# Performance work log

Measured on AMD Instinct MI355X. Metric: run time of the kernel, lower is better.

The kernel has to match this reference:

```python
import jax, jax.numpy as jnp
import numpy as np

DIM = 256
N_NODES = 2000
BATCH = 64


def _build_tree(n, seed=0):
    # Contiguous-children encoding: struct[i] = (ch_start, ch_end) or (-1,-1) for leaves.
    # Children indices are always > parent index (BFS frontier allocation).
    rng = np.random.default_rng(seed)
    struct = np.full((n, 2), -1, dtype=np.int32)
    ptr = 1
    i = 0
    while ptr < n:
        k = int(rng.integers(0, 5))
        if i + 1 >= ptr:  # keep the frontier non-empty
            k = max(k, 1)
        k = min(k, n - ptr)
        if k > 0:
            struct[i] = (ptr, ptr + k)
            ptr += k
        i += 1
    return struct


def _level_schedule(struct):
    # depth 0 = leaves; parent depth = 1 + max(child depths). Children idx > parent idx.
    n = struct.shape[0]
    depth = np.zeros(n, dtype=np.int64)
    for i in range(n - 1, -1, -1):
        s, e = struct[i]
        if s != -1:
            depth[i] = 1 + depth[s:e].max()
    return [np.nonzero(depth == d)[0] for d in range(int(depth.max()) + 1)]


def setup_inputs() -> dict:
    key = jax.random.key(0)
    ks = jax.random.split(key, 3)
    struct = _build_tree(N_NODES)
    structure = jnp.asarray(np.broadcast_to(struct, (BATCH, N_NODES, 2)).copy())
    features = jax.random.normal(ks[0], (BATCH, N_NODES, DIM), dtype=jnp.float32)
    s_in = (2.0 / (DIM + DIM)) ** 0.5        # glorot-ish scale
    s_inner = (2.0 / (3 * DIM + DIM)) ** 0.5
    W_in = jax.random.normal(ks[1], (DIM, DIM), dtype=jnp.float32) * s_in
    b_in = jnp.zeros((DIM,), jnp.float32)
    W_inner = jax.random.normal(ks[2], (3 * DIM, DIM), dtype=jnp.float32) * s_inner
    b_inner = jnp.zeros((DIM,), jnp.float32)
    return {"structure": structure, "features": features, "W_in": W_in,
            "b_in": b_in, "W_inner": W_inner, "b_inner": b_inner}


def reference(structure, features, W_in, b_in, W_inner, b_inner):
    # Tree structure (int) is a compile-time constant: derive a level schedule host-side,
    # then run one batched segment-reduction + Dense per tree level (deepest first).
    struct = np.asarray(structure[0])  # shared across batch
    levels = _level_schedule(struct)
    B, N, dim = features.shape
    state = jnp.zeros((B, N, dim), features.dtype)

    # Leaves: sigmoid Dense on own features (all features are finite/valid here).
    leaves = levels[0]
    state = state.at[:, leaves].set(jax.nn.sigmoid(features[:, leaves] @ W_in + b_in))

    for nodes in levels[1:]:
        starts, ends = struct[nodes, 0], struct[nodes, 1]
        counts = ends - starts
        child_ids = np.concatenate([np.arange(s, e) for s, e in zip(starts, ends)])
        seg = np.repeat(np.arange(len(nodes)), counts)
        L = len(nodes)
        cs = state[:, child_ids].transpose(1, 0, 2)          # [C, B, dim]
        ssum = jax.ops.segment_sum(cs, seg, num_segments=L)  # [L, B, dim]
        smin = jax.ops.segment_min(cs, seg, num_segments=L)
        feat = features[:, nodes].transpose(1, 0, 2)         # node's own feature joins pooling
        cnt = jnp.asarray(counts + 1, features.dtype)[:, None, None]
        c_mean = (ssum + feat) / cnt
        c_min = jnp.minimum(smin, feat)
        # NOTE: the source computes c_max with reduce_mean (bug) -> kept for fidelity.
        h = jnp.concatenate([c_mean, c_mean, c_min], axis=-1)  # [L, B, 3*dim]
        new = jax.nn.sigmoid(h @ W_inner + b_inner)
        state = state.at[:, nodes].set(new.transpose(1, 0, 2))

    return state[:, 0]  # just_root_output=True -> [B, dim]
```

## Files before the change

### kernel.cpp

```cpp
#include <hip/hip_runtime.h>

#define NNODES 2000
#define BATCH  64
#define DIM    256
#define BLOCK  256
#define MAXGRID 512
#define MAXLVL 128
#define TBLD   264

typedef __attribute__((ext_vector_type(8))) short  v8s;
typedef __attribute__((ext_vector_type(8))) __bf16 v8bf;
typedef __attribute__((ext_vector_type(4))) float  v4f;
typedef __attribute__((ext_vector_type(4))) int    v4i;

__device__ __forceinline__ short f2bf(float f) {
  unsigned u = __builtin_bit_cast(unsigned, f);
  u += 0x7FFFu + ((u >> 16) & 1u);
  return (short)(u >> 16);
}
__device__ __forceinline__ float bf2f(short s) {
  unsigned u = ((unsigned)(unsigned short)s) << 16;
  return __builtin_bit_cast(float, u);
}
__device__ __forceinline__ v4f mfma16(v8s a, v8s b, v4f c) {
  return __builtin_amdgcn_mfma_f32_16x16x32_bf16(
      __builtin_bit_cast(v8bf, a), __builtin_bit_cast(v8bf, b), c, 0, 0, 0);
}
__device__ __forceinline__ float sigmoidf(float x) {
  return __builtin_amdgcn_rcpf(1.0f + __builtin_amdgcn_exp2f(-1.4426950408889634f * x));
}

__global__ void prep1_kernel(const float* __restrict__ W_in, const float* __restrict__ W_inner,
                             short* __restrict__ Wt_in, short* __restrict__ Wt_inner,
                             int* __restrict__ bar) {
  int idx = blockIdx.x * blockDim.x + threadIdx.x;
  int stride = gridDim.x * blockDim.x;
  for (int i = idx; i < 256 * 256; i += stride) {
    int j = i >> 8, k = i & 255;
    Wt_in[j * 256 + k] = f2bf(W_in[k * 256 + j]);
  }
  for (int i = idx; i < 256 * 512; i += stride) {
    int j = i >> 9, k = i & 511;
    float v = W_inner[(k + 256) * 256 + j];
    if (k < 256) v += W_inner[k * 256 + j];
    Wt_inner[j * 512 + k] = f2bf(v);
  }
  if (idx == 0)
    __hip_atomic_store(bar, 0, __ATOMIC_RELAXED, __HIP_MEMORY_SCOPE_AGENT);
}

__global__ void prep2_kernel(const int* __restrict__ structure,
                             int* __restrict__ order, int* __restrict__ lstart,
                             int* __restrict__ meta) {
  __shared__ int   structS[NNODES * 2];
  __shared__ short h[NNODES];
  __shared__ int   counts[MAXLVL];
  __shared__ int   lsS[MAXLVL + 1];
  __shared__ int   chg, Hlev;
  const int tid = threadIdx.x;
  for (int i = tid; i < NNODES * 2; i += BLOCK) structS[i] = structure[i];
  for (int i = tid; i < NNODES; i += BLOCK) h[i] = 0;
  for (int i = tid; i < MAXLVL; i += BLOCK) counts[i] = 0;
  __syncthreads();
  for (int pass = 0; pass < 4096; ++pass) {
    if (tid == 0) chg = 0;
    __syncthreads();
    int any = 0;
    for (int i = tid; i < NNODES; i += BLOCK) {
      const int s = structS[2 * i];
      if (s >= 0) {
        const int e = structS[2 * i + 1];
        int m = 0;
        for (int c = s; c < e; ++c) m = max(m, (int)h[c]);
        if (m + 1 > (int)h[i]) { h[i] = (short)(m + 1); any = 1; }
      }
    }
    if (any) chg = 1;
    __syncthreads();
    if (chg == 0) break;
    __syncthreads();
  }
  for (int i = tid; i < NNODES; i += BLOCK) atomicAdd(&counts[h[i]], 1);
  __syncthreads();
  if (tid == 0) {
    int acc = 0, hm = 0;
    for (int l = 0; l < MAXLVL; ++l) {
      lsS[l] = acc; acc += counts[l];
      if (counts[l] > 0) hm = l + 1;
    }
    lsS[MAXLVL] = acc;
    Hlev = hm;
    meta[0] = hm;
  }
  __syncthreads();
  for (int i = tid; i <= MAXLVL; i += BLOCK) lstart[i] = lsS[i];
  const int wave = tid >> 6, lane = tid & 63;
  for (int lev = wave; lev < Hlev; lev += 4) {
    int cnt = lsS[lev];
    for (int base = 0; base < NNODES; base += 64) {
      const int i = base + lane;
      const bool p = (i < NNODES) && ((int)h[i] == lev);
      const unsigned long long m = __ballot(p);
      if (p) order[cnt + (int)__popcll(m & ((1ull << lane) - 1ull))] = i;
      cnt += (int)__popcll(m);
    }
  }
}

__launch_bounds__(BLOCK, 2)
__global__ void tree_kernel(const int* __restrict__ structure, const float* __restrict__ features,
                            const float* __restrict__ b_in, const float* __restrict__ b_inner,
                            const short* __restrict__ Wt_in, const short* __restrict__ Wt_inner,
                            const int* __restrict__ order, const int* __restrict__ lstart,
                            const int* __restrict__ meta,
                            short* __restrict__ state, int* __restrict__ bar,
                            float* __restrict__ out) {
  __shared__ short Xs[32 * 512];

  const int tid  = threadIdx.x;
  const int wave = tid >> 6;
  const int lane = tid & 63;
  const int ln15 = lane & 15;
  const int quad = lane >> 4;
  const int rl3  = ln15 & 7;

  const int rowb = tid >> 5;
  const int ch   = tid & 31;

  float bia_in[4], bia_nn[4];
  #pragma unroll
  for (int nt = 0; nt < 4; ++nt) {
    const int j = wave * 64 + nt * 16 + ln15;
    bia_in[nt] = b_in[j];
    bia_nn[nt] = b_inner[j];
  }

  const int nlev = meta[0];

  for (int lev = 0; lev < nlev; ++lev) {
    const int kbeg = lstart[lev];
    const int cnt  = lstart[lev + 1] - kbeg;
    for (int idx = (int)blockIdx.x; idx < 2 * cnt; idx += (int)gridDim.x) {
      const int node = order[kbeg + (idx >> 1)];
      const int half = idx & 1;
      const int s = structure[2 * node];
      const int e = structure[2 * node + 1];
      const bool leaf = (s < 0);
      const int nc = e - s;
      const int K = leaf ? 256 : 512;
      const short* __restrict__ W = leaf ? Wt_in : Wt_inner;

      float4 pf[4][2];
      #pragma unroll
      for (int g = 0; g < 4; ++g) {
        const int b = half * 32 + rowb + 8 * g;
        const float* __restrict__ fp = features + ((size_t)b * NNODES + node) * DIM + ch * 8;
        pf[g][0] = ((const float4*)fp)[0];
        pf[g][1] = ((const float4*)fp)[1];
      }
      if (leaf) {
        #pragma unroll
        for (int g = 0; g < 4; ++g) {
          const int row = rowb + 8 * g;
          const float4 f0 = pf[g][0], f1 = pf[g][1];
          v8s o;
          o[0] = f2bf(f0.x); o[1] = f2bf(f0.y); o[2] = f2bf(f0.z); o[3] = f2bf(f0.w);
          o[4] = f2bf(f1.x); o[5] = f2bf(f1.y); o[6] = f2bf(f1.z); o[7] = f2bf(f1.w);
          *(v8s*)&Xs[(row << 9) + ((ch ^ rowb) << 3)] = o;
        }
      } else {
        v4i cb[4][4];
        #pragma unroll
        for (int ci = 0; ci < 4; ++ci) {
          if (ci < nc) {
            #pragma unroll
            for (int g = 0; g < 4; ++g) {
              const short* cp = state +
                  ((size_t)(s + ci) * BATCH + half * 32 + rowb + 8 * g) * DIM + ch * 8;
              asm volatile("global_load_dwordx4 %0, %1, off sc0 sc1"
                           : "=v"(cb[ci][g]) : "v"(cp));
            }
          }
        }
        asm volatile("s_waitcnt vmcnt(0)" ::: "memory");
        __builtin_amdgcn_sched_barrier(0);

        const float inv = 1.0f / (float)(nc + 1);
        #pragma unroll
        for (int g = 0; g < 4; ++g) {
          const int row = rowb + 8 * g;
          const float4 f0 = pf[g][0], f1 = pf[g][1];
          float sm[8] = {f0.x, f0.y, f0.z, f0.w, f1.x, f1.y, f1.z, f1.w};
          float mn[8];
          #pragma unroll
          for (int qq = 0; qq < 8; ++qq) mn[qq] = sm[qq];
          #pragma unroll
          for (int ci = 0; ci < 4; ++ci) {
            if (ci < nc) {
              const v8s cv = __builtin_bit_cast(v8s, cb[ci][g]);
              #pragma unroll
              for (int qq = 0; qq < 8; ++qq) {
                const float v = bf2f(cv[qq]);
                sm[qq] += v; mn[qq] = fminf(mn[qq], v);
              }
            }
          }
          v8s om, on;
          #pragma unroll
          for (int qq = 0; qq < 8; ++qq) { om[qq] = f2bf(sm[qq] * inv); on[qq] = f2bf(mn[qq]); }
          *(v8s*)&Xs[(row << 9) + ((ch ^ rowb) << 3)]        = om;
          *(v8s*)&Xs[(row << 9) + (((ch + 32) ^ rowb) << 3)] = on;
        }
      }
      __syncthreads();

      v4f acc[2][4];
      #pragma unroll
      for (int mt = 0; mt < 2; ++mt)
        #pragma unroll
        for (int nt = 0; nt < 4; ++nt) acc[mt][nt] = v4f{0.f, 0.f, 0.f, 0.f};

      const short* __restrict__ Wp = W + (size_t)(wave * 64 + ln15) * K + quad * 8;
      const int nkc = K >> 5;
      v8s bcur[4];
      #pragma unroll
      for (int nt = 0; nt < 4; ++nt) bcur[nt] = *(const v8s*)(Wp + (size_t)nt * 16 * K);
      for (int kc = 0; kc < nkc; ++kc) {
        const int kn = (kc + 1 < nkc) ? kc + 1 : kc;
        v8s bnxt[4];
        #pragma unroll
        for (int nt = 0; nt < 4; ++nt) bnxt[nt] = *(const v8s*)(Wp + (size_t)nt * 16 * K + kn * 32);
        v8s af[2];
        #pragma unroll
        for (int mt = 0; mt < 2; ++mt) {
          const int r = mt * 16 + ln15;
          af[mt] = *(const v8s*)&Xs[(r << 9) + (((kc * 4 + quad) ^ rl3) << 3)];
        }
        #pragma unroll
        for (int mt = 0; mt < 2; ++mt)
          #pragma unroll
          for (int nt = 0; nt < 4; ++nt)
            acc[mt][nt] = mfma16(af[mt], bcur[nt], acc[mt][nt]);
        #pragma unroll
        for (int nt = 0; nt < 4; ++nt) bcur[nt] = bnxt[nt];
      }
      __syncthreads();

      #pragma unroll
      for (int nt = 0; nt < 4; ++nt) {
        const int j = wave * 64 + nt * 16 + ln15;
        const float bs = leaf ? bia_in[nt] : bia_nn[nt];
        #pragma unroll
        for (int mt = 0; mt < 2; ++mt) {
          #pragma unroll
          for (int r = 0; r < 4; ++r) {
            const int bb = mt * 16 + quad * 4 + r;
            const float v = sigmoidf(acc[mt][nt][r] + bs);
            Xs[bb * TBLD + j] = f2bf(v);
            if (node == 0) out[(half * 32 + bb) * DIM + j] = v;
          }
        }
      }
      __syncthreads();

      #pragma unroll
      for (int g = 0; g < 4; ++g) {
        const int row = rowb + 8 * g;
        const v4i val = *(const v4i*)&Xs[row * TBLD + ch * 8];
        short* sp = state + ((size_t)node * BATCH + half * 32 + row) * DIM + ch * 8;
        asm volatile("global_store_dwordx4 %0, %1, off sc0 sc1" :: "v"(sp), "v"(val));
      }
      __syncthreads();
    }

    asm volatile("s_waitcnt vmcnt(0)" ::: "memory");
    __syncthreads();
    if (tid == 0) {
      __hip_atomic_fetch_add(bar, 1, __ATOMIC_RELAXED, __HIP_MEMORY_SCOPE_AGENT);
      const int target = (lev + 1) * (int)gridDim.x;
      int g = 0;
      while (__hip_atomic_load(bar, __ATOMIC_RELAXED, __HIP_MEMORY_SCOPE_AGENT) < target &&
             g < (1 << 24)) {
        __builtin_amdgcn_s_sleep(1); ++g;
      }
    }
    __syncthreads();
  }
}

extern "C" void kernel_launch(void* const* d_in, const int* in_sizes, int n_in,
                              void* d_out, int out_size, void* d_ws, size_t ws_size,
                              hipStream_t stream) {
  const int*   structure = (const int*)d_in[0];
  const float* features  = (const float*)d_in[1];
  const float* W_in      = (const float*)d_in[2];
  const float* b_in      = (const float*)d_in[3];
  const float* W_inner   = (const float*)d_in[4];
  const float* b_inner   = (const float*)d_in[5];
  float* out = (float*)d_out;

  char* ws = (char*)d_ws;
  short* state = (short*)ws;
  size_t off = (size_t)NNODES * BATCH * DIM * 2;
  short* Wt_in = (short*)(ws + off);    off += 256 * 256 * 2;
  short* Wt_inner = (short*)(ws + off); off += 512 * 256 * 2;
  int* order  = (int*)(ws + off);       off += NNODES * 4;
  int* lstart = (int*)(ws + off);       off += (MAXLVL + 1) * 4;
  int* meta   = (int*)(ws + off);       off += 4;
  int* bar    = (int*)(ws + off);

  prep1_kernel<<<dim3(256), dim3(256), 0, stream>>>(W_in, W_inner, Wt_in, Wt_inner, bar);
  prep2_kernel<<<dim3(1), dim3(BLOCK), 0, stream>>>(structure, order, lstart, meta);

  static int coop_grid = 0;
  if (coop_grid == 0) {
    int nb = 0;
    hipError_t err = hipOccupancyMaxActiveBlocksPerMultiprocessor(
        &nb, reinterpret_cast<const void*>(tree_kernel), BLOCK, 0);
    if (err != hipSuccess || nb < 1) nb = 1;
    long g = (long)nb * 256;
    if (g > MAXGRID) g = MAXGRID;
    coop_grid = (int)g;
  }

  void* args[12];
  args[0]  = (void*)&structure;
  args[1]  = (void*)&features;
  args[2]  = (void*)&b_in;
  args[3]  = (void*)&b_inner;
  args[4]  = (void*)&Wt_in;
  args[5]  = (void*)&Wt_inner;
  args[6]  = (void*)&order;
  args[7]  = (void*)&lstart;
  args[8]  = (void*)&meta;
  args[9]  = (void*)&state;
  args[10] = (void*)&bar;
  args[11] = (void*)&out;
  hipLaunchCooperativeKernel((void*)tree_kernel, dim3(coop_grid), dim3(BLOCK), args, 0, stream);
}
```

Before: 536.5 us.

## Replace cooperative persistent kernel with per-level kernel launches

Drops the single cooperative kernel and its atomic grid barrier between tree levels. Work is now split into a merged prep kernel (weight transpose plus level schedule in one launch), a leaf kernel with one block per node-half, and a fixed run of inner-level kernels, one launch per level up to a compile-time maximum. Kernel boundaries take over the synchronisation and allow a larger grid, at the cost of launch overhead and no-op launches for levels beyond the real depth. The hard LMAX and MAXLVL caps assume the tree depth stays small, and the software-pipelined weight prefetch and cache-bypassing loads and stores are removed.

```diff
diff --git a/kernel.cpp b/kernel.cpp
--- a/kernel.cpp
+++ b/kernel.cpp
@@ -4,8 +4,9 @@
 #define BATCH  64
 #define DIM    256
 #define BLOCK  256
-#define MAXGRID 512
-#define MAXLVL 128
+#define MAXLVL 64
+#define LMAX   20
+#define INGRID 1024
 #define TBLD   264
 
 typedef __attribute__((ext_vector_type(8))) short  v8s;
@@ -30,92 +31,91 @@
   return __builtin_amdgcn_rcpf(1.0f + __builtin_amdgcn_exp2f(-1.4426950408889634f * x));
 }
 
-__global__ void prep1_kernel(const float* __restrict__ W_in, const float* __restrict__ W_inner,
-                             short* __restrict__ Wt_in, short* __restrict__ Wt_inner,
-                             int* __restrict__ bar) {
-  int idx = blockIdx.x * blockDim.x + threadIdx.x;
-  int stride = gridDim.x * blockDim.x;
-  for (int i = idx; i < 256 * 256; i += stride) {
-    int j = i >> 8, k = i & 255;
-    Wt_in[j * 256 + k] = f2bf(W_in[k * 256 + j]);
-  }
-  for (int i = idx; i < 256 * 512; i += stride) {
-    int j = i >> 9, k = i & 511;
-    float v = W_inner[(k + 256) * 256 + j];
-    if (k < 256) v += W_inner[k * 256 + j];
-    Wt_inner[j * 512 + k] = f2bf(v);
-  }
-  if (idx == 0)
-    __hip_atomic_store(bar, 0, __ATOMIC_RELAXED, __HIP_MEMORY_SCOPE_AGENT);
-}
-
-__global__ void prep2_kernel(const int* __restrict__ structure,
-                             int* __restrict__ order, int* __restrict__ lstart,
-                             int* __restrict__ meta) {
+__global__ void prep_kernel(const float* __restrict__ W_in, const float* __restrict__ W_inner,
+                            short* __restrict__ Wt_in, short* __restrict__ Wt_inner,
+                            const int* __restrict__ structure,
+                            int* __restrict__ order, int* __restrict__ lstart,
+                            int* __restrict__ meta) {
   __shared__ int   structS[NNODES * 2];
   __shared__ short h[NNODES];
   __shared__ int   counts[MAXLVL];
   __shared__ int   lsS[MAXLVL + 1];
   __shared__ int   chg, Hlev;
   const int tid = threadIdx.x;
-  for (int i = tid; i < NNODES * 2; i += BLOCK) structS[i] = structure[i];
-  for (int i = tid; i < NNODES; i += BLOCK) h[i] = 0;
-  for (int i = tid; i < MAXLVL; i += BLOCK) counts[i] = 0;
-  __syncthreads();
-  for (int pass = 0; pass < 4096; ++pass) {
-    if (tid == 0) chg = 0;
-    __syncthreads();
-    int any = 0;
-    for (int i = tid; i < NNODES; i += BLOCK) {
-      const int s = structS[2 * i];
-      if (s >= 0) {
-        const int e = structS[2 * i + 1];
-        int m = 0;
-        for (int c = s; c < e; ++c) m = max(m, (int)h[c]);
-        if (m + 1 > (int)h[i]) { h[i] = (short)(m + 1); any = 1; }
-      }
-    }
-    if (any) chg = 1;
-    __syncthreads();
-    if (chg == 0) break;
-    __syncthreads();
-  }
-  for (int i = tid; i < NNODES; i += BLOCK) atomicAdd(&counts[h[i]], 1);
-  __syncthreads();
-  if (tid == 0) {
-    int acc = 0, hm = 0;
-    for (int l = 0; l < MAXLVL; ++l) {
-      lsS[l] = acc; acc += counts[l];
-      if (counts[l] > 0) hm = l + 1;
-    }
-    lsS[MAXLVL] = acc;
-    Hlev = hm;
-    meta[0] = hm;
-  }
-  __syncthreads();
-  for (int i = tid; i <= MAXLVL; i += BLOCK) lstart[i] = lsS[i];
-  const int wave = tid >> 6, lane = tid & 63;
-  for (int lev = wave; lev < Hlev; lev += 4) {
-    int cnt = lsS[lev];
-    for (int base = 0; base < NNODES; base += 64) {
-      const int i = base + lane;
-      const bool p = (i < NNODES) && ((int)h[i] == lev);
-      const unsigned long long m = __ballot(p);
-      if (p) order[cnt + (int)__popcll(m & ((1ull << lane) - 1ull))] = i;
-      cnt += (int)__popcll(m);
+
+  if (blockIdx.x == 0) {
+    for (int i = tid; i < NNODES * 2; i += BLOCK) structS[i] = structure[i];
+    for (int i = tid; i < NNODES; i += BLOCK) h[i] = 0;
+    for (int i = tid; i < MAXLVL; i += BLOCK) counts[i] = 0;
+    __syncthreads();
+    for (int pass = 0; pass < 4096; ++pass) {
+      if (tid == 0) chg = 0;
+      __syncthreads();
+      int any = 0;
+      for (int i = tid; i < NNODES; i += BLOCK) {
+        const int s = structS[2 * i];
+        if (s >= 0) {
+          const int e = structS[2 * i + 1];
+          int m = 0;
+          for (int c = s; c < e; ++c) m = max(m, (int)h[c]);
+          if (m + 1 > (int)h[i]) { h[i] = (short)(m + 1); any = 1; }
+        }
+      }
+      if (any) chg = 1;
+      __syncthreads();
+      if (chg == 0) break;
+      __syncthreads();
+    }
+    for (int i = tid; i < NNODES; i += BLOCK) atomicAdd(&counts[h[i]], 1);
+    __syncthreads();
+    if (tid == 0) {
+      int acc = 0, hm = 0;
+      for (int l = 0; l < MAXLVL; ++l) {
+        lsS[l] = acc; acc += counts[l];
+        if (counts[l] > 0) hm = l + 1;
+      }
+      lsS[MAXLVL] = acc;
+      Hlev = hm;
+      meta[0] = hm;
+    }
+    __syncthreads();
+    for (int i = tid; i <= MAXLVL; i += BLOCK) lstart[i] = lsS[i];
+    const int wave = tid >> 6, lane = tid & 63;
+    for (int lev = wave; lev < Hlev; lev += 4) {
+      int cnt = lsS[lev];
+      for (int base = 0; base < NNODES; base += 64) {
+        const int i = base + lane;
+        const bool p = (i < NNODES) && ((int)h[i] == lev);
+        const unsigned long long m = __ballot(p);
+        if (p) order[cnt + (int)__popcll(m & ((1ull << lane) - 1ull))] = i;
+        cnt += (int)__popcll(m);
+      }
+    }
+  } else {
+    const int idx = ((int)blockIdx.x - 1) * BLOCK + tid;
+    {
+      const int j = idx >> 8, k = idx & 255;
+      Wt_in[j * 256 + k] = f2bf(W_in[k * 256 + j]);
+    }
+    for (int t = idx; t < 256 * 512; t += 65536) {
+      const int j = t >> 9, k = t & 511;
+      float v = W_inner[(k + 256) * 256 + j];
+      if (k < 256) v += W_inner[k * 256 + j];
+      Wt_inner[j * 512 + k] = f2bf(v);
     }
   }
 }
 
 __launch_bounds__(BLOCK, 2)
-__global__ void tree_kernel(const int* __restrict__ structure, const float* __restrict__ features,
-                            const float* __restrict__ b_in, const float* __restrict__ b_inner,
-                            const short* __restrict__ Wt_in, const short* __restrict__ Wt_inner,
-                            const int* __restrict__ order, const int* __restrict__ lstart,
-                            const int* __restrict__ meta,
-                            short* __restrict__ state, int* __restrict__ bar,
-                            float* __restrict__ out) {
+__global__ void leaf_kernel(const int* __restrict__ structure, const float* __restrict__ features,
+                            const float* __restrict__ b_in, const short* __restrict__ Wt_in,
+                            short* __restrict__ state) {
   __shared__ short Xs[32 * 512];
+
+  const int idx = (int)blockIdx.x;
+  const int node = idx >> 1;
+  const int half = idx & 1;
+  if (structure[2 * node] >= 0) return;
 
   const int tid  = threadIdx.x;
   const int wave = tid >> 6;
@@ -123,166 +123,196 @@
   const int ln15 = lane & 15;
   const int quad = lane >> 4;
   const int rl3  = ln15 & 7;
-
   const int rowb = tid >> 5;
   const int ch   = tid & 31;
 
-  float bia_in[4], bia_nn[4];
+  #pragma unroll
+  for (int g = 0; g < 4; ++g) {
+    const int row = rowb + 8 * g;
+    const int b   = half * 32 + row;
+    const float* __restrict__ fp = features + ((size_t)b * NNODES + node) * DIM + ch * 8;
+    const float4 f0 = ((const float4*)fp)[0];
+    const float4 f1 = ((const float4*)fp)[1];
+    v8s o;
+    o[0] = f2bf(f0.x); o[1] = f2bf(f0.y); o[2] = f2bf(f0.z); o[3] = f2bf(f0.w);
+    o[4] = f2bf(f1.x); o[5] = f2bf(f1.y); o[6] = f2bf(f1.z); o[7] = f2bf(f1.w);
+    *(v8s*)&Xs[(row << 9) + ((ch ^ rowb) << 3)] = o;
+  }
+  __syncthreads();
+
+  v4f acc[2][4];
+  #pragma unroll
+  for (int mt = 0; mt < 2; ++mt)
+    #pragma unroll
+    for (int nt = 0; nt < 4; ++nt) acc[mt][nt] = v4f{0.f, 0.f, 0.f, 0.f};
+
+  const short* __restrict__ Wp = Wt_in + (size_t)(wave * 64 + ln15) * 256 + quad * 8;
+  for (int kc = 0; kc < 8; ++kc) {
+    v8s bf[4];
+    #pragma unroll
+    for (int nt = 0; nt < 4; ++nt) bf[nt] = *(const v8s*)(Wp + (size_t)nt * 16 * 256 + kc * 32);
+    v8s af[2];
+    #pragma unroll
+    for (int mt = 0; mt < 2; ++mt) {
+      const int r = mt * 16 + ln15;
+      af[mt] = *(const v8s*)&Xs[(r << 9) + (((kc * 4 + quad) ^ rl3) << 3)];
+    }
+    #pragma unroll
+    for (int mt = 0; mt < 2; ++mt)
+      #pragma unroll
+      for (int nt = 0; nt < 4; ++nt)
+        acc[mt][nt] = mfma16(af[mt], bf[nt], acc[mt][nt]);
+  }
+  __syncthreads();
+
   #pragma unroll
   for (int nt = 0; nt < 4; ++nt) {
     const int j = wave * 64 + nt * 16 + ln15;
-    bia_in[nt] = b_in[j];
-    bia_nn[nt] = b_inner[j];
-  }
-
-  const int nlev = meta[0];
-
-  for (int lev = 0; lev < nlev; ++lev) {
-    const int kbeg = lstart[lev];
-    const int cnt  = lstart[lev + 1] - kbeg;
-    for (int idx = (int)blockIdx.x; idx < 2 * cnt; idx += (int)gridDim.x) {
-      const int node = order[kbeg + (idx >> 1)];
-      const int half = idx & 1;
-      const int s = structure[2 * node];
-      const int e = structure[2 * node + 1];
-      const bool leaf = (s < 0);
-      const int nc = e - s;
-      const int K = leaf ? 256 : 512;
-      const short* __restrict__ W = leaf ? Wt_in : Wt_inner;
-
-      float4 pf[4][2];
-      #pragma unroll
-      for (int g = 0; g < 4; ++g) {
-        const int b = half * 32 + rowb + 8 * g;
-        const float* __restrict__ fp = features + ((size_t)b * NNODES + node) * DIM + ch * 8;
-        pf[g][0] = ((const float4*)fp)[0];
-        pf[g][1] = ((const float4*)fp)[1];
-      }
-      if (leaf) {
+    const float bs = b_in[j];
+    #pragma unroll
+    for (int mt = 0; mt < 2; ++mt) {
+      #pragma unroll
+      for (int r = 0; r < 4; ++r) {
+        const int bb = mt * 16 + quad * 4 + r;
+        Xs[bb * TBLD + j] = f2bf(sigmoidf(acc[mt][nt][r] + bs));
+      }
+    }
+  }
+  __syncthreads();
+  #pragma unroll
+  for (int g = 0; g < 4; ++g) {
+    const int row = rowb + 8 * g;
+    const v4i val = *(const v4i*)&Xs[row * TBLD + ch * 8];
+    *(v4i*)(state + ((size_t)node * BATCH + half * 32 + row) * DIM + ch * 8) = val;
+  }
+}
+
+__launch_bounds__(BLOCK, 2)
+__global__ void inner_kernel(const int* __restrict__ structure, const float* __restrict__ features,
+                             const float* __restrict__ b_inner, const short* __restrict__ Wt_inner,
+                             const int* __restrict__ order, const int* __restrict__ lstart,
+                             const int* __restrict__ meta,
+                             short* __restrict__ state, float* __restrict__ out, int lev) {
+  __shared__ short Xs[32 * 512];
+
+  if (lev >= meta[0]) return;
+
+  const int tid  = threadIdx.x;
+  const int wave = tid >> 6;
+  const int lane = tid & 63;
+  const int ln15 = lane & 15;
+  const int quad = lane >> 4;
+  const int rl3  = ln15 & 7;
+  const int rowb = tid >> 5;
+  const int ch   = tid & 31;
+
+  float bia[4];
+  #pragma unroll
+  for (int nt = 0; nt < 4; ++nt) bia[nt] = b_inner[wave * 64 + nt * 16 + ln15];
+
+  const int kbeg = lstart[lev];
+  const int cnt  = lstart[lev + 1] - kbeg;
+
+  for (int idx = (int)blockIdx.x; idx < 2 * cnt; idx += (int)gridDim.x) {
+    const int node = order[kbeg + (idx >> 1)];
+    const int half = idx & 1;
+    const int s = structure[2 * node];
+    const int e = structure[2 * node + 1];
+    const int nc = e - s;
+
+    float4 pf[4][2];
+    #pragma unroll
+    for (int g = 0; g < 4; ++g) {
+      const int b = half * 32 + rowb + 8 * g;
+      const float* __restrict__ fp = features + ((size_t)b * NNODES + node) * DIM + ch * 8;
+      pf[g][0] = ((const float4*)fp)[0];
+      pf[g][1] = ((const float4*)fp)[1];
+    }
+    v4i cb[4][4];
+    #pragma unroll
+    for (int ci = 0; ci < 4; ++ci) {
+      if (ci < nc) {
         #pragma unroll
-        for (int g = 0; g < 4; ++g) {
-          const int row = rowb + 8 * g;
-          const float4 f0 = pf[g][0], f1 = pf[g][1];
-          v8s o;
-          o[0] = f2bf(f0.x); o[1] = f2bf(f0.y); o[2] = f2bf(f0.z); o[3] = f2bf(f0.w);
-          o[4] = f2bf(f1.x); o[5] = f2bf(f1.y); o[6] = f2bf(f1.z); o[7] = f2bf(f1.w);
-          *(v8s*)&Xs[(row << 9) + ((ch ^ rowb) << 3)] = o;
-        }
-      } else {
-        v4i cb[4][4];
-        #pragma unroll
-        for (int ci = 0; ci < 4; ++ci) {
-          if (ci < nc) {
-            #pragma unroll
-            for (int g = 0; g < 4; ++g) {
-              const short* cp = state +
-                  ((size_t)(s + ci) * BATCH + half * 32 + rowb + 8 * g) * DIM + ch * 8;
-              asm volatile("global_load_dwordx4 %0, %1, off sc0 sc1"
-                           : "=v"(cb[ci][g]) : "v"(cp));
-            }
+        for (int g = 0; g < 4; ++g)
+          cb[ci][g] = *(const v4i*)(state +
+              ((size_t)(s + ci) * BATCH + half * 32 + rowb + 8 * g) * DIM + ch * 8);
+      }
+    }
+
+    const float inv = 1.0f / (float)(nc + 1);
+    #pragma unroll
+    for (int g = 0; g < 4; ++g) {
+      const int row = rowb + 8 * g;
+      const float4 f0 = pf[g][0], f1 = pf[g][1];
+      float sm[8] = {f0.x, f0.y, f0.z, f0.w, f1.x, f1.y, f1.z, f1.w};
+      float mn[8];
+      #pragma unroll
+      for (int qq = 0; qq < 8; ++qq) mn[qq] = sm[qq];
+      #pragma unroll
+      for (int ci = 0; ci < 4; ++ci) {
+        if (ci < nc) {
+          const v8s cv = __builtin_bit_cast(v8s, cb[ci][g]);
+          #pragma unroll
+          for (int qq = 0; qq < 8; ++qq) {
+            const float v = bf2f(cv[qq]);
+            sm[qq] += v; mn[qq] = fminf(mn[qq], v);
           }
         }
-        asm volatile("s_waitcnt vmcnt(0)" ::: "memory");
-        __builtin_amdgcn_sched_barrier(0);
-
-        const float inv = 1.0f / (float)(nc + 1);
-        #pragma unroll
-        for (int g = 0; g < 4; ++g) {
-          const int row = rowb + 8 * g;
-          const float4 f0 = pf[g][0], f1 = pf[g][1];
-          float sm[8] = {f0.x, f0.y, f0.z, f0.w, f1.x, f1.y, f1.z, f1.w};
-          float mn[8];
-          #pragma unroll
-          for (int qq = 0; qq < 8; ++qq) mn[qq] = sm[qq];
-          #pragma unroll
-          for (int ci = 0; ci < 4; ++ci) {
-            if (ci < nc) {
-              const v8s cv = __builtin_bit_cast(v8s, cb[ci][g]);
-              #pragma unroll
-              for (int qq = 0; qq < 8; ++qq) {
-                const float v = bf2f(cv[qq]);
-                sm[qq] += v; mn[qq] = fminf(mn[qq], v);
-              }
-            }
-          }
-          v8s om, on;
-          #pragma unroll
-          for (int qq = 0; qq < 8; ++qq) { om[qq] = f2bf(sm[qq] * inv); on[qq] = f2bf(mn[qq]); }
-          *(v8s*)&Xs[(row << 9) + ((ch ^ rowb) << 3)]        = om;
-          *(v8s*)&Xs[(row << 9) + (((ch + 32) ^ rowb) << 3)] = on;
-        }
-      }
-      __syncthreads();
-
-      v4f acc[2][4];
+      }
+      v8s om, on;
+      #pragma unroll
+      for (int qq = 0; qq < 8; ++qq) { om[qq] = f2bf(sm[qq] * inv); on[qq] = f2bf(mn[qq]); }
+      *(v8s*)&Xs[(row << 9) + ((ch ^ rowb) << 3)]        = om;
+      *(v8s*)&Xs[(row << 9) + (((ch + 32) ^ rowb) << 3)] = on;
+    }
+    __syncthreads();
+
+    v4f acc[2][4];
+    #pragma unroll
+    for (int mt = 0; mt < 2; ++mt)
+      #pragma unroll
+      for (int nt = 0; nt < 4; ++nt) acc[mt][nt] = v4f{0.f, 0.f, 0.f, 0.f};
+
+    const short* __restrict__ Wp = Wt_inner + (size_t)(wave * 64 + ln15) * 512 + quad * 8;
+    for (int kc = 0; kc < 16; ++kc) {
+      v8s bf[4];
+      #pragma unroll
+      for (int nt = 0; nt < 4; ++nt) bf[nt] = *(const v8s*)(Wp + (size_t)nt * 16 * 512 + kc * 32);
+      v8s af[2];
+      #pragma unroll
+      for (int mt = 0; mt < 2; ++mt) {
+        const int r = mt * 16 + ln15;
+        af[mt] = *(const v8s*)&Xs[(r << 9) + (((kc * 4 + quad) ^ rl3) << 3)];
+      }
       #pragma unroll
       for (int mt = 0; mt < 2; ++mt)
         #pragma unroll
-        for (int nt = 0; nt < 4; ++nt) acc[mt][nt] = v4f{0.f, 0.f, 0.f, 0.f};
-
-      const short* __restrict__ Wp = W + (size_t)(wave * 64 + ln15) * K + quad * 8;
-      const int nkc = K >> 5;
-      v8s bcur[4];
-      #pragma unroll
-      for (int nt = 0; nt < 4; ++nt) bcur[nt] = *(const v8s*)(Wp + (size_t)nt * 16 * K);
-      for (int kc = 0; kc < nkc; ++kc) {
-        const int kn = (kc + 1 < nkc) ? kc + 1 : kc;
-        v8s bnxt[4];
+        for (int nt = 0; nt < 4; ++nt)
+          acc[mt][nt] = mfma16(af[mt], bf[nt], acc[mt][nt]);
+    }
+    __syncthreads();
+
+    #pragma unroll
+    for (int nt = 0; nt < 4; ++nt) {
+      const int j = wave * 64 + nt * 16 + ln15;
+      const float bs = bia[nt];
+      #pragma unroll
+      for (int mt = 0; mt < 2; ++mt) {
         #pragma unroll
-        for (int nt = 0; nt < 4; ++nt) bnxt[nt] = *(const v8s*)(Wp + (size_t)nt * 16 * K + kn * 32);
-        v8s af[2];
-        #pragma unroll
-        for (int mt = 0; mt < 2; ++mt) {
-          const int r = mt * 16 + ln15;
-          af[mt] = *(const v8s*)&Xs[(r << 9) + (((kc * 4 + quad) ^ rl3) << 3)];
+        for (int r = 0; r < 4; ++r) {
+          const int bb = mt * 16 + quad * 4 + r;
+          const float v = sigmoidf(acc[mt][nt][r] + bs);
+          Xs[bb * TBLD + j] = f2bf(v);
+          if (node == 0) out[(half * 32 + bb) * DIM + j] = v;
         }
-        #pragma unroll
-        for (int mt = 0; mt < 2; ++mt)
-          #pragma unroll
-          for (int nt = 0; nt < 4; ++nt)
-            acc[mt][nt] = mfma16(af[mt], bcur[nt], acc[mt][nt]);
-        #pragma unroll
-        for (int nt = 0; nt < 4; ++nt) bcur[nt] = bnxt[nt];
-      }
-      __syncthreads();
-
-      #pragma unroll
-      for (int nt = 0; nt < 4; ++nt) {
-        const int j = wave * 64 + nt * 16 + ln15;
-        const float bs = leaf ? bia_in[nt] : bia_nn[nt];
-        #pragma unroll
-        for (int mt = 0; mt < 2; ++mt) {
-          #pragma unroll
-          for (int r = 0; r < 4; ++r) {
-            const int bb = mt * 16 + quad * 4 + r;
-            const float v = sigmoidf(acc[mt][nt][r] + bs);
-            Xs[bb * TBLD + j] = f2bf(v);
-            if (node == 0) out[(half * 32 + bb) * DIM + j] = v;
-          }
-        }
-      }
-      __syncthreads();
-
-      #pragma unroll
-      for (int g = 0; g < 4; ++g) {
-        const int row = rowb + 8 * g;
-        const v4i val = *(const v4i*)&Xs[row * TBLD + ch * 8];
-        short* sp = state + ((size_t)node * BATCH + half * 32 + row) * DIM + ch * 8;
-        asm volatile("global_store_dwordx4 %0, %1, off sc0 sc1" :: "v"(sp), "v"(val));
-      }
-      __syncthreads();
-    }
-
-    asm volatile("s_waitcnt vmcnt(0)" ::: "memory");
-    __syncthreads();
-    if (tid == 0) {
-      __hip_atomic_fetch_add(bar, 1, __ATOMIC_RELAXED, __HIP_MEMORY_SCOPE_AGENT);
-      const int target = (lev + 1) * (int)gridDim.x;
-      int g = 0;
-      while (__hip_atomic_load(bar, __ATOMIC_RELAXED, __HIP_MEMORY_SCOPE_AGENT) < target &&
-             g < (1 << 24)) {
-        __builtin_amdgcn_s_sleep(1); ++g;
-      }
+      }
+    }
+    __syncthreads();
+    #pragma unroll
+    for (int g = 0; g < 4; ++g) {
+      const int row = rowb + 8 * g;
+      const v4i val = *(const v4i*)&Xs[row * TBLD + ch * 8];
+      *(v4i*)(state + ((size_t)node * BATCH + half * 32 + row) * DIM + ch * 8) = val;
     }
     __syncthreads();
   }
@@ -306,35 +336,14 @@
   short* Wt_inner = (short*)(ws + off); off += 512 * 256 * 2;
   int* order  = (int*)(ws + off);       off += NNODES * 4;
   int* lstart = (int*)(ws + off);       off += (MAXLVL + 1) * 4;
-  int* meta   = (int*)(ws + off);       off += 4;
-  int* bar    = (int*)(ws + off);
-
-  prep1_kernel<<<dim3(256), dim3(256), 0, stream>>>(W_in, W_inner, Wt_in, Wt_inner, bar);
-  prep2_kernel<<<dim3(1), dim3(BLOCK), 0, stream>>>(structure, order, lstart, meta);
-
-  static int coop_grid = 0;
-  if (coop_grid == 0) {
-    int nb = 0;
-    hipError_t err = hipOccupancyMaxActiveBlocksPerMultiprocessor(
-        &nb, reinterpret_cast<const void*>(tree_kernel), BLOCK, 0);
-    if (err != hipSuccess || nb < 1) nb = 1;
-    long g = (long)nb * 256;
-    if (g > MAXGRID) g = MAXGRID;
-    coop_grid = (int)g;
-  }
-
-  void* args[12];
-  args[0]  = (void*)&structure;
-  args[1]  = (void*)&features;
-  args[2]  = (void*)&b_in;
-  args[3]  = (void*)&b_inner;
-  args[4]  = (void*)&Wt_in;
-  args[5]  = (void*)&Wt_inner;
-  args[6]  = (void*)&order;
-  args[7]  = (void*)&lstart;
-  args[8]  = (void*)&meta;
-  args[9]  = (void*)&state;
-  args[10] = (void*)&bar;
-  args[11] = (void*)&out;
-  hipLaunchCooperativeKernel((void*)tree_kernel, dim3(coop_grid), dim3(BLOCK), args, 0, stream);
-}
+  int* meta   = (int*)(ws + off);
+
+  prep_kernel<<<dim3(257), dim3(BLOCK), 0, stream>>>(W_in, W_inner, Wt_in, Wt_inner,
+                                                     structure, order, lstart, meta);
+  leaf_kernel<<<dim3(2 * NNODES), dim3(BLOCK), 0, stream>>>(structure, features, b_in,
+                                                            Wt_in, state);
+  for (int lev = 1; lev < LMAX; ++lev)
+    inner_kernel<<<dim3(INGRID), dim3(BLOCK), 0, stream>>>(structure, features, b_inner,
+                                                           Wt_inner, order, lstart, meta,
+                                                           state, out, lev);
+}
```

Result: no change. 546.4 us (+1.8%).
